# Kernel tuning notes

Hardware: AMD Instinct MI355X
Metric: run time of the kernel (lower is better)

## Reference

```python
import jax, jax.numpy as jnp
import numpy as np

B, S, SIZE1 = 128, 1024, 64
N, SIZE0 = 2048, 512


def setup_inputs() -> dict:
    key = jax.random.key(0)
    k1, k2, k3, k4 = jax.random.split(key, 4)
    encoder_outputs = jax.random.normal(k1, (B, S, SIZE1), dtype=jnp.float32)
    encoder_outputs_neighbor = jax.random.normal(k2, (B, N, SIZE0), dtype=jnp.float32)
    # nn.Linear(size0, size1) parameters
    W = jax.random.normal(k3, (SIZE1, SIZE0), dtype=jnp.float32) / np.sqrt(SIZE0)
    b = jax.random.normal(k4, (SIZE1,), dtype=jnp.float32) * 0.01
    return {
        "encoder_outputs": encoder_outputs,
        "current_index": 100,
        "encoder_outputs_neighbor": encoder_outputs_neighbor,
        "neighbor_num": N,
        "W": W,
        "b": b,
    }


def reference(encoder_outputs, current_index, encoder_outputs_neighbor, neighbor_num, W, b):
    # temp: query vector per batch element, [B, size1]
    temp = encoder_outputs[:, current_index, :]
    # batched linear projection: [B, N, size0] -> [B, N, size1]
    energy = jnp.einsum("bns,ds->bnd", encoder_outputs_neighbor, W) + b
    # diag(energy[k] @ temp_copy) == rowwise dot product with temp[k]
    attn_energies = jnp.einsum("bnd,bd->bn", energy, temp)  # [B, N]
    return jax.nn.softmax(attn_energies, axis=1)
```

## Files before the change

kernel.cpp:

```cpp
#include <hip/hip_runtime.h>
#include <hip/hip_bf16.h>
#include <math.h>

#define B_   128
#define S_   1024
#define D1_  64
#define N_   2048
#define D0_  512

__global__ __launch_bounds__(D0_) void prep_kernel(
    const float* __restrict__ enc, const int* __restrict__ cur_idx,
    const float* __restrict__ W, float* __restrict__ v)
{
    __shared__ float temp[D1_];
    const int b = blockIdx.x;
    const int t = threadIdx.x;
    const int ci = *cur_idx;
    if (t < D1_) {
        temp[t] = enc[(size_t)b * (S_ * D1_) + (size_t)ci * D1_ + t];
    }
    __syncthreads();
    float acc = 0.f;
#pragma unroll
    for (int d = 0; d < D1_; ++d) {
        acc += temp[d] * W[d * D0_ + t];
    }
    v[b * D0_ + t] = acc;
}

__global__ __launch_bounds__(256) void logits_kernel(
    const float* __restrict__ nb, const float* __restrict__ v,
    float* __restrict__ out)
{
    const int wave = threadIdx.x >> 6;
    const int lane = threadIdx.x & 63;
    const size_t row = (size_t)blockIdx.x * 4 + wave;
    const int b = (int)(row >> 11);
    const float4* __restrict__ r = (const float4*)(nb + row * D0_);
    const float4* __restrict__ vv = (const float4*)(v + (size_t)b * D0_);

    float4 r0 = r[lane];
    float4 r1 = r[lane + 64];
    float4 v0 = vv[lane];
    float4 v1 = vv[lane + 64];

    float s = r0.x * v0.x + r0.y * v0.y + r0.z * v0.z + r0.w * v0.w
            + r1.x * v1.x + r1.y * v1.y + r1.z * v1.z + r1.w * v1.w;

#pragma unroll
    for (int off = 32; off; off >>= 1) s += __shfl_xor(s, off);

    if (lane == 0) out[row] = s;
}

__global__ __launch_bounds__(256) void softmax_kernel(float* __restrict__ out)
{
    float* row = out + (size_t)blockIdx.x * N_;
    const int t = threadIdx.x;
    const int wave = t >> 6, lane = t & 63;

    float vals[8];
    float m = -INFINITY;
#pragma unroll
    for (int i = 0; i < 8; ++i) {
        vals[i] = row[t + i * 256];
        m = fmaxf(m, vals[i]);
    }
#pragma unroll
    for (int off = 32; off; off >>= 1) m = fmaxf(m, __shfl_xor(m, off));

    __shared__ float redm[4];
    __shared__ float reds[4];
    if (lane == 0) redm[wave] = m;
    __syncthreads();
    m = fmaxf(fmaxf(redm[0], redm[1]), fmaxf(redm[2], redm[3]));

    float s = 0.f;
#pragma unroll
    for (int i = 0; i < 8; ++i) {
        vals[i] = __expf(vals[i] - m);
        s += vals[i];
    }
#pragma unroll
    for (int off = 32; off; off >>= 1) s += __shfl_xor(s, off);
    if (lane == 0) reds[wave] = s;
    __syncthreads();
    s = reds[0] + reds[1] + reds[2] + reds[3];

    const float inv = 1.0f / s;
#pragma unroll
    for (int i = 0; i < 8; ++i) row[t + i * 256] = vals[i] * inv;
}

extern "C" void kernel_launch(void* const* d_in, const int* in_sizes, int n_in,
                              void* d_out, int out_size, void* d_ws, size_t ws_size,
                              hipStream_t stream)
{
    const float* enc     = (const float*)d_in[0];
    const int*   cur_idx = (const int*)d_in[1];
    const float* nb      = (const float*)d_in[2];
    const float* W       = (const float*)d_in[4];
    float*       out     = (float*)d_out;
    float*       v       = (float*)d_ws;

    prep_kernel<<<B_, D0_, 0, stream>>>(enc, cur_idx, W, v);
    logits_kernel<<<(B_ * N_) / 4, 256, 0, stream>>>(nb, v, out);
    softmax_kernel<<<B_, 256, 0, stream>>>(out);
}
```

Baseline: 95.06 us.

## Compute one logit row per thread with query vector staged in LDS

Rewrites the logits kernel so each thread computes a full 512-element dot product for one neighbor row, reading the projected query from shared memory instead of using a wave-wide shuffle reduction per row. Blocks now cover 256 rows of one batch element, and the grid shrinks accordingly. This removes the cross-lane reduction and repeated global loads of v, but adjacent threads now read addresses 2KB apart, making global loads uncoalesced and raising cache and TLB pressure.

```diff
diff --git a/kernel.cpp b/kernel.cpp
--- a/kernel.cpp
+++ b/kernel.cpp
@@ -32,25 +32,26 @@
     const float* __restrict__ nb, const float* __restrict__ v,
     float* __restrict__ out)
 {
-    const int wave = threadIdx.x >> 6;
-    const int lane = threadIdx.x & 63;
-    const size_t row = (size_t)blockIdx.x * 4 + wave;
-    const int b = (int)(row >> 11);
+    __shared__ float4 vs[D0_ / 4];
+    const int t = threadIdx.x;
+    const int b = blockIdx.x >> 3;
+
+    if (t < D0_ / 4) {
+        vs[t] = ((const float4*)(v + (size_t)b * D0_))[t];
+    }
+    __syncthreads();
+
+    const size_t row = (size_t)blockIdx.x * 256 + t;
     const float4* __restrict__ r = (const float4*)(nb + row * D0_);
-    const float4* __restrict__ vv = (const float4*)(v + (size_t)b * D0_);
 
-    float4 r0 = r[lane];
-    float4 r1 = r[lane + 64];
-    float4 v0 = vv[lane];
-    float4 v1 = vv[lane + 64];
-
-    float s = r0.x * v0.x + r0.y * v0.y + r0.z * v0.z + r0.w * v0.w
-            + r1.x * v1.x + r1.y * v1.y + r1.z * v1.z + r1.w * v1.w;
-
-#pragma unroll
-    for (int off = 32; off; off >>= 1) s += __shfl_xor(s, off);
-
-    if (lane == 0) out[row] = s;
+    float acc = 0.f;
+#pragma unroll 16
+    for (int k = 0; k < D0_ / 4; ++k) {
+        const float4 a = r[k];
+        const float4 w = vs[k];
+        acc += a.x * w.x + a.y * w.y + a.z * w.z + a.w * w.w;
+    }
+    out[row] = acc;
 }
 
 __global__ __launch_bounds__(256) void softmax_kernel(float* __restrict__ out)
@@ -104,6 +105,6 @@
     float*       v       = (float*)d_ws;
 
     prep_kernel<<<B_, D0_, 0, stream>>>(enc, cur_idx, W, v);
-    logits_kernel<<<(B_ * N_) / 4, 256, 0, stream>>>(nb, v, out);
+    logits_kernel<<<(B_ * N_) / 256, 256, 0, stream>>>(nb, v, out);
     softmax_kernel<<<B_, 256, 0, stream>>>(out);
 }
```

Measured after the change: 134.6 us. +41.6%, slower.
